# Kernel optimization log

Measured on AMD Instinct MI355X. Metric: run time of the kernel, lower is better.

## Reference

```python
import jax, jax.numpy as jnp
import numpy as np

B, T, H, DFF = 32, 4096, 512, 512  # hidden_size=512, d_ff=512, h feature dim = 2*H


def setup_inputs() -> dict:
    key = jax.random.key(0)
    ks = jax.random.split(key, 8)
    sc = 0.02
    return {
        "s": jax.random.normal(ks[0], (B, H), dtype=jnp.float32),
        "h": jax.random.normal(ks[1], (B, T, 2 * H), dtype=jnp.float32),
        "W_a_w": jax.random.normal(ks[2], (DFF, H), dtype=jnp.float32) * sc,
        "W_a_b": jnp.zeros((DFF,), dtype=jnp.float32),
        "U_a_w": jax.random.normal(ks[3], (DFF, 2 * H), dtype=jnp.float32) * sc,
        "U_a_b": jnp.zeros((DFF,), dtype=jnp.float32),
        "V_a_w": jax.random.normal(ks[4], (1, DFF), dtype=jnp.float32) * sc,
        "V_a_b": jnp.zeros((1,), dtype=jnp.float32),
    }


def reference(s, h, W_a_w, W_a_b, U_a_w, U_a_b, V_a_w, V_a_b):
    # Bahdanau additive attention scoring (NOTE: original has no softmax).
    ws = s @ W_a_w.T + W_a_b                              # [B, d_ff]
    uh = jnp.einsum('bte,fe->btf', h, U_a_w) + U_a_b       # [B, T, d_ff]
    x = jnp.tanh(ws[:, None, :] + uh)                      # [B, T, d_ff]
    energy = x @ V_a_w[0] + V_a_b[0]                       # [B, T]
    context = jnp.einsum('bt,bte->be', energy, h)          # [B, 2*hidden]
    return context
```

## Files before the change

kernel.cpp:

```cpp
#include <hip/hip_runtime.h>
#include <cstdint>
#include <cstddef>

#define B_SZ 32
#define T_SZ 4096
#define H2   1024
#define DFF_ 512
#define TM   64
#define BK   32
#define NSTEP (H2 / BK)

typedef __attribute__((ext_vector_type(8))) short bf16x8;
typedef __attribute__((ext_vector_type(4))) float f32x4;

__device__ __forceinline__ unsigned short f2bf(float x) {
  unsigned u = __float_as_uint(x);
  u += 0x7fffu + ((u >> 16) & 1u);
  return (unsigned short)(u >> 16);
}

__global__ void prep_u_kernel(const float* __restrict__ U,
                              unsigned short* __restrict__ Upk) {
  int g = blockIdx.x * 256 + threadIdx.x;
  int j  = g & 7;
  int l  = (g >> 3) & 63;
  int ct = (g >> 9) & 31;
  int ks = g >> 14;
  int f  = ct * 16 + (l & 15);
  int k  = ks * 32 + (l >> 4) * 8 + j;
  Upk[g] = f2bf(U[f * H2 + k]);
}

__global__ void prep_ws_kernel(const float* __restrict__ s, const float* __restrict__ W,
                               const float* __restrict__ Wb, const float* __restrict__ Ub,
                               float* __restrict__ wsm) {
  int idx = blockIdx.x * 256 + threadIdx.x;
  int b = idx >> 9, f = idx & 511;
  const float4* s4 = (const float4*)(s + b * 512);
  const float4* w4 = (const float4*)(W + f * 512);
  float acc = 0.f;
  #pragma unroll 4
  for (int i = 0; i < 128; ++i) {
    float4 a = s4[i], w = w4[i];
    acc += a.x * w.x + a.y * w.y + a.z * w.z + a.w * w.w;
  }
  wsm[idx] = acc + Wb[f] + Ub[f];
}

__global__ __launch_bounds__(512, 4) void attn_main(
    const float* __restrict__ h, const unsigned short* __restrict__ Upk,
    const float* __restrict__ wsm, const float* __restrict__ Vw,
    const float* __restrict__ Vb, float* __restrict__ out) {
  __shared__ unsigned short Bs[2][NSTEP ? 32 * 64 * 8 : 1];
  __shared__ unsigned short As[2][4 * 64 * 8];
  __shared__ float ws_s[DFF_];
  __shared__ float V_s[DFF_];
  __shared__ float energy_part[8][TM];
  __shared__ float energy_s[TM];

  const int tid  = threadIdx.x;
  const int blk  = blockIdx.x;
  const int b    = blk >> 6;
  const int t0   = (blk & 63) * TM;
  const int lane = tid & 63;
  const int cg   = tid >> 6;
  const int ln15 = lane & 15;
  const int q4   = lane >> 4;

  ws_s[tid] = wsm[b * DFF_ + tid];
  V_s[tid]  = Vw[tid];

  const int arow = tid >> 3;
  const int ak   = (tid & 7) * 4;
  const int a_off = (arow >> 4) * 512 + (ak >> 3) * 128 + (arow & 15) * 8 + (ak & 7);
  const float* hbase = h + ((size_t)(b * T_SZ + t0)) * H2;
  const float* aptr  = hbase + (size_t)arow * H2 + ak;

  f32x4 acc[16];
  #pragma unroll
  for (int i = 0; i < 16; ++i) acc[i] = (f32x4){0.f, 0.f, 0.f, 0.f};

  auto stageB = [&](int ks, int buf) {
    const char* gsrc = (const char*)Upk + (size_t)ks * 32768;
    char* ldst = (char*)&Bs[buf][0];
    #pragma unroll
    for (int i = 0; i < 4; ++i) {
      int off = i * 8192 + tid * 16;
      __builtin_amdgcn_global_load_lds(
        (const __attribute__((address_space(1))) unsigned int*)(gsrc + off),
        (__attribute__((address_space(3))) unsigned int*)(ldst + off),
        16, 0, 0);
    }
  };
  auto writeA = [&](float4 av, int buf) {
    ushort4 ab;
    ab.x = f2bf(av.x); ab.y = f2bf(av.y); ab.z = f2bf(av.z); ab.w = f2bf(av.w);
    *(ushort4*)&As[buf][a_off] = ab;
  };

  stageB(0, 0);
  {
    float4 av0 = *(const float4*)(aptr);
    writeA(av0, 0);
  }
  __syncthreads();

  for (int ks = 0; ks < NSTEP; ++ks) {
    const int cur = ks & 1;
    float4 av;
    if (ks < NSTEP - 1) {
      stageB(ks + 1, cur ^ 1);
      av = *(const float4*)(aptr + (ks + 1) * BK);
    }
    bf16x8 af[4];
    #pragma unroll
    for (int rt = 0; rt < 4; ++rt)
      af[rt] = *(const bf16x8*)&As[cur][rt * 512 + lane * 8];
    #pragma unroll
    for (int ct2 = 0; ct2 < 4; ++ct2) {
      int ct = cg * 4 + ct2;
      bf16x8 bfr = *(const bf16x8*)&Bs[cur][(ct * 64 + lane) * 8];
      #pragma unroll
      for (int rt = 0; rt < 4; ++rt)
        acc[ct2 * 4 + rt] =
          __builtin_amdgcn_mfma_f32_16x16x32_bf16(af[rt], bfr, acc[ct2 * 4 + rt], 0, 0, 0);
    }
    if (ks < NSTEP - 1) writeA(av, cur ^ 1);
    __syncthreads();
  }

  float esum[16];
  #pragma unroll
  for (int i = 0; i < 16; ++i) esum[i] = 0.f;
  #pragma unroll
  for (int ct2 = 0; ct2 < 4; ++ct2) {
    int f = cg * 64 + ct2 * 16 + ln15;
    float wsf = ws_s[f], vf = V_s[f];
    #pragma unroll
    for (int rt = 0; rt < 4; ++rt) {
      #pragma unroll
      for (int rg = 0; rg < 4; ++rg) {
        float z = wsf + acc[ct2 * 4 + rt][rg];
        float e = __expf(2.f * z);
        float x = 1.f - 2.f / (e + 1.f);
        esum[rt * 4 + rg] += x * vf;
      }
    }
  }
  #pragma unroll
  for (int i = 0; i < 16; ++i) {
    #pragma unroll
    for (int m = 1; m < 16; m <<= 1) esum[i] += __shfl_xor(esum[i], m, 64);
  }
  if (ln15 == 0) {
    #pragma unroll
    for (int rt = 0; rt < 4; ++rt)
      #pragma unroll
      for (int rg = 0; rg < 4; ++rg)
        energy_part[cg][rt * 16 + q4 * 4 + rg] = esum[rt * 4 + rg];
  }
  __syncthreads();
  if (tid < TM) {
    float e = Vb[0];
    #pragma unroll
    for (int w = 0; w < 8; ++w) e += energy_part[w][tid];
    energy_s[tid] = e;
  }
  __syncthreads();

  int e0 = tid * 2;
  float c0 = 0.f, c1 = 0.f;
  const float2* h2p = (const float2*)hbase + (e0 >> 1);
  #pragma unroll 4
  for (int row = 0; row < TM; ++row) {
    float en = energy_s[row];
    float2 hv = h2p[(size_t)row * (H2 / 2)];
    c0 += en * hv.x;
    c1 += en * hv.y;
  }
  atomicAdd(&out[b * H2 + e0], c0);
  atomicAdd(&out[b * H2 + e0 + 1], c1);
}

extern "C" void kernel_launch(void* const* d_in, const int* in_sizes, int n_in,
                              void* d_out, int out_size, void* d_ws, size_t ws_size,
                              hipStream_t stream) {
  const float* s  = (const float*)d_in[0];
  const float* h  = (const float*)d_in[1];
  const float* Ww = (const float*)d_in[2];
  const float* Wb = (const float*)d_in[3];
  const float* Uw = (const float*)d_in[4];
  const float* Ub = (const float*)d_in[5];
  const float* Vw = (const float*)d_in[6];
  const float* Vb = (const float*)d_in[7];
  float* out = (float*)d_out;

  unsigned short* Upk = (unsigned short*)d_ws;
  float* wsm = (float*)((char*)d_ws + (size_t)NSTEP * 32768);

  hipMemsetAsync(out, 0, (size_t)out_size * sizeof(float), stream);
  prep_u_kernel<<<(DFF_ * H2) / 256, 256, 0, stream>>>(Uw, Upk);
  prep_ws_kernel<<<(B_SZ * DFF_) / 256, 256, 0, stream>>>(s, Ww, Wb, Ub, wsm);
  attn_main<<<B_SZ * (T_SZ / TM), 512, 0, stream>>>(h, Upk, wsm, Vw, Vb, out);
}
```

Baseline: 899.3 us.

## Stage half of h tile in LDS at once and stream U fragments via registers

```diff
diff --git a/kernel.cpp b/kernel.cpp
--- a/kernel.cpp
+++ b/kernel.cpp
@@ -8,7 +8,8 @@
 #define DFF_ 512
 #define TM   64
 #define BK   32
-#define NSTEP (H2 / BK)
+#define SPH  16
+#define NSTEP 32
 
 typedef __attribute__((ext_vector_type(8))) short bf16x8;
 typedef __attribute__((ext_vector_type(4))) float f32x4;
@@ -51,8 +52,7 @@
     const float* __restrict__ h, const unsigned short* __restrict__ Upk,
     const float* __restrict__ wsm, const float* __restrict__ Vw,
     const float* __restrict__ Vb, float* __restrict__ out) {
-  __shared__ unsigned short Bs[2][NSTEP ? 32 * 64 * 8 : 1];
-  __shared__ unsigned short As[2][4 * 64 * 8];
+  __shared__ unsigned short As[SPH * 2048];
   __shared__ float ws_s[DFF_];
   __shared__ float V_s[DFF_];
   __shared__ float energy_part[8][TM];
@@ -74,59 +74,65 @@
   const int ak   = (tid & 7) * 4;
   const int a_off = (arow >> 4) * 512 + (ak >> 3) * 128 + (arow & 15) * 8 + (ak & 7);
   const float* hbase = h + ((size_t)(b * T_SZ + t0)) * H2;
-  const float* aptr  = hbase + (size_t)arow * H2 + ak;
+  const float* hrow  = hbase + (size_t)arow * H2 + ak;
+
+  const bf16x8* Upk8 = (const bf16x8*)Upk;
 
   f32x4 acc[16];
   #pragma unroll
   for (int i = 0; i < 16; ++i) acc[i] = (f32x4){0.f, 0.f, 0.f, 0.f};
 
-  auto stageB = [&](int ks, int buf) {
-    const char* gsrc = (const char*)Upk + (size_t)ks * 32768;
-    char* ldst = (char*)&Bs[buf][0];
-    #pragma unroll
-    for (int i = 0; i < 4; ++i) {
-      int off = i * 8192 + tid * 16;
-      __builtin_amdgcn_global_load_lds(
-        (const __attribute__((address_space(1))) unsigned int*)(gsrc + off),
-        (__attribute__((address_space(3))) unsigned int*)(ldst + off),
-        16, 0, 0);
-    }
-  };
-  auto writeA = [&](float4 av, int buf) {
-    ushort4 ab;
-    ab.x = f2bf(av.x); ab.y = f2bf(av.y); ab.z = f2bf(av.z); ab.w = f2bf(av.w);
-    *(ushort4*)&As[buf][a_off] = ab;
-  };
-
-  stageB(0, 0);
-  {
-    float4 av0 = *(const float4*)(aptr);
-    writeA(av0, 0);
-  }
-  __syncthreads();
-
-  for (int ks = 0; ks < NSTEP; ++ks) {
-    const int cur = ks & 1;
-    float4 av;
-    if (ks < NSTEP - 1) {
-      stageB(ks + 1, cur ^ 1);
-      av = *(const float4*)(aptr + (ks + 1) * BK);
-    }
-    bf16x8 af[4];
-    #pragma unroll
-    for (int rt = 0; rt < 4; ++rt)
-      af[rt] = *(const bf16x8*)&As[cur][rt * 512 + lane * 8];
-    #pragma unroll
-    for (int ct2 = 0; ct2 < 4; ++ct2) {
-      int ct = cg * 4 + ct2;
-      bf16x8 bfr = *(const bf16x8*)&Bs[cur][(ct * 64 + lane) * 8];
+  for (int hk = 0; hk < 2; ++hk) {
+    if (hk) __syncthreads();
+    {
+      float4 avv[8];
+      #pragma unroll
+      for (int j = 0; j < 8; ++j) avv[j] = *(const float4*)(hrow + hk * 512 + j * BK);
+      #pragma unroll
+      for (int j = 0; j < 8; ++j) {
+        ushort4 ab;
+        ab.x = f2bf(avv[j].x); ab.y = f2bf(avv[j].y);
+        ab.z = f2bf(avv[j].z); ab.w = f2bf(avv[j].w);
+        *(ushort4*)&As[j * 2048 + a_off] = ab;
+      }
+      #pragma unroll
+      for (int j = 0; j < 8; ++j) avv[j] = *(const float4*)(hrow + hk * 512 + (j + 8) * BK);
+      #pragma unroll
+      for (int j = 0; j < 8; ++j) {
+        ushort4 ab;
+        ab.x = f2bf(avv[j].x); ab.y = f2bf(avv[j].y);
+        ab.z = f2bf(avv[j].z); ab.w = f2bf(avv[j].w);
+        *(ushort4*)&As[(j + 8) * 2048 + a_off] = ab;
+      }
+    }
+    __syncthreads();
+    const int ksbase = hk * SPH;
+    bf16x8 bcur[4], bnxt[4];
+    {
+      size_t base = ((size_t)(ksbase * 32 + cg * 4)) * 64 + lane;
+      #pragma unroll
+      for (int i = 0; i < 4; ++i) bcur[i] = Upk8[base + (size_t)i * 64];
+    }
+    #pragma unroll
+    for (int s = 0; s < SPH; ++s) {
+      if (s < SPH - 1) {
+        size_t base = ((size_t)((ksbase + s + 1) * 32 + cg * 4)) * 64 + lane;
+        #pragma unroll
+        for (int i = 0; i < 4; ++i) bnxt[i] = Upk8[base + (size_t)i * 64];
+      }
+      bf16x8 af[4];
       #pragma unroll
       for (int rt = 0; rt < 4; ++rt)
-        acc[ct2 * 4 + rt] =
-          __builtin_amdgcn_mfma_f32_16x16x32_bf16(af[rt], bfr, acc[ct2 * 4 + rt], 0, 0, 0);
-    }
-    if (ks < NSTEP - 1) writeA(av, cur ^ 1);
-    __syncthreads();
+        af[rt] = *(const bf16x8*)&As[s * 2048 + rt * 512 + lane * 8];
+      #pragma unroll
+      for (int ct2 = 0; ct2 < 4; ++ct2)
+        #pragma unroll
+        for (int rt = 0; rt < 4; ++rt)
+          acc[ct2 * 4 + rt] =
+            __builtin_amdgcn_mfma_f32_16x16x32_bf16(af[rt], bcur[ct2], acc[ct2 * 4 + rt], 0, 0, 0);
+      #pragma unroll
+      for (int i = 0; i < 4; ++i) bcur[i] = bnxt[i];
+    }
   }
 
   float esum[16];
```

Result: no change. 886.7 us (-1.4%).
